# Kernel tuning notes

Hardware: AMD Instinct MI355X
Metric: run time of the kernel (lower is better)

Reference implementation:

```python
import jax, jax.numpy as jnp
import numpy as np

N, L, LEADS = 512, 640, 3
COND_DIM, NUM_K, DIM_K = 1, 100, 5
FLAT = 256 * 79  # 20224, from conv stack trace


def _leaky(x):
    return jnp.where(x >= 0, x, 0.2 * x)


def _sn(w, u):
    # PyTorch spectral_norm: one power iteration (u, v detached), sigma = u^T W v
    wm = w.reshape(w.shape[0], -1)
    v = wm.T @ u
    v = v / (jnp.linalg.norm(v) + 1e-12)
    u2 = wm @ v
    u2 = u2 / (jnp.linalg.norm(u2) + 1e-12)
    u2 = jax.lax.stop_gradient(u2)
    v = jax.lax.stop_gradient(v)
    sigma = u2 @ (wm @ v)
    return w / sigma


def _conv1d(x, w, b, stride, pad):
    y = jax.lax.conv_general_dilated(
        x, w, window_strides=(stride,), padding=[(pad, pad)],
        dimension_numbers=('NCH', 'OIH', 'NCH'))
    return y + b[None, :, None]


def setup_inputs() -> dict:
    key = jax.random.key(0)
    ks = jax.random.split(key, 16)
    g = lambda k, shp, s: (jax.random.normal(k, shp, dtype=jnp.float32) * s)
    inp = {
        'ecg': jax.random.normal(ks[0], (N, L, LEADS), dtype=jnp.float32),
        'condition': jax.random.randint(ks[1], (N, 1), 0, 4),
        'w1': g(ks[2], (64, LEADS, 5), 0.2), 'b1': jnp.zeros((64,), jnp.float32),
        'u1': jax.random.normal(ks[3], (64,), dtype=jnp.float32),
        'w2': g(ks[4], (128, 64, 7), 0.05), 'b2': jnp.zeros((128,), jnp.float32),
        'u2': jax.random.normal(ks[5], (128,), dtype=jnp.float32),
        'w3': g(ks[6], (256, 128, 9), 0.03), 'b3': jnp.zeros((256,), jnp.float32),
        'u3': jax.random.normal(ks[7], (256,), dtype=jnp.float32),
        'emb': g(ks[8], (4, COND_DIM), 1.0),
        'cond_w': g(ks[9], (50, COND_DIM), 0.5), 'cond_b': jnp.zeros((50,), jnp.float32),
        'mb_w': g(ks[10], (FLAT, NUM_K * DIM_K), 0.01),
        'fc_w': g(ks[11], (1, FLAT + NUM_K + 50), 0.01), 'fc_b': jnp.zeros((1,), jnp.float32),
    }
    return inp


def reference(ecg, condition, w1, b1, u1, w2, b2, u2, w3, b3, u3,
              emb, cond_w, cond_b, mb_w, fc_w, fc_b):
    # condition embedding -> Linear(cond_dim, 50)
    cemb = emb[condition[:, 0]]                       # [N, cond_dim]
    cond = cemb @ cond_w.T + cond_b                   # [N, 50]

    x = ecg.transpose(0, 2, 1)                        # [N, 3, 640]
    x = _leaky(_conv1d(x, _sn(w1, u1), b1, 2, 4))     # [N, 64, 322]
    x = _leaky(_conv1d(x, _sn(w2, u2), b2, 2, 3))     # [N, 128, 161]
    x = _leaky(_conv1d(x, _sn(w3, u3), b3, 2, 2))     # [N, 256, 79]
    flat = x.reshape(x.shape[0], -1)                  # [N, 20224]

    # minibatch discrimination
    act = (flat @ mb_w).reshape(-1, NUM_K, DIM_K)     # [N, K, D]
    l1 = jnp.abs(act[:, None] - act[None, :]).sum(-1)  # [N, N, K]
    feats = jnp.exp(-l1).sum(axis=1)                  # [N, K]

    out = jnp.concatenate([flat, feats, cond], axis=1)
    return out @ fc_w.T + fc_b                        # [N, 1]
```

## Files before the change

kernel.cpp:

```cpp
#include <hip/hip_runtime.h>
#include <math.h>

#define NB 512
#define LIN 640
#define NLEADS 3
#define L1O 322
#define L2O 161
#define L3O 79
#define C1N 64
#define C2N 128
#define C3N 256
#define FLATSZ 20224
#define NUMK 100
#define DIMK 5
#define SPLITK 16

typedef __attribute__((ext_vector_type(8))) short short8;
typedef __attribute__((ext_vector_type(4))) float f32x4;

__device__ __forceinline__ unsigned short f2bf(float x){
  unsigned u = __builtin_bit_cast(unsigned, x);
  unsigned r = u + 0x7FFFu + ((u >> 16) & 1u);
  return (unsigned short)(r >> 16);
}
__device__ __forceinline__ float bf2f(unsigned short x){
  unsigned u = ((unsigned)x) << 16;
  return __builtin_bit_cast(float, u);
}

__device__ __forceinline__ float block_reduce_sum(float val, float* red){
#pragma unroll
  for(int off=32; off>0; off>>=1) val += __shfl_down(val, off, 64);
  int lane = threadIdx.x & 63;
  int wv = threadIdx.x >> 6;
  if(lane==0) red[wv] = val;
  __syncthreads();
  int nw = blockDim.x >> 6;
  float r = red[0];
  for(int i=1;i<nw;i++) r += red[i];
  __syncthreads();
  return r;
}

__global__ __launch_bounds__(256)
void sn_pass1(const float* __restrict__ w1, const float* __restrict__ u1,
              const float* __restrict__ w2, const float* __restrict__ u2,
              const float* __restrict__ w3, const float* __restrict__ u3,
              float* __restrict__ v_all, float* __restrict__ ss){
  __shared__ float red[4];
  int b = blockIdx.x, tid = threadIdx.x;
  const float* w; const float* u; int O, C, off, c, widx;
  if(b==0){ w=w1; u=u1; O=64;  C=15;   off=0;   c=tid;            widx=0; }
  else if(b<3){ w=w2; u=u2; O=128; C=448; off=16;  c=(b-1)*256+tid; widx=1; }
  else { w=w3; u=u3; O=256; C=1152; off=464; c=(b-3)*256+tid;      widx=2; }
  float vv = 0.f;
  if(c < C){
    for(int o=0;o<O;o+=4){
      vv += w[(o+0)*C+c]*u[o+0] + w[(o+1)*C+c]*u[o+1]
          + w[(o+2)*C+c]*u[o+2] + w[(o+3)*C+c]*u[o+3];
    }
    v_all[off + c] = vv;
  }
  float ps = (c < C) ? vv*vv : 0.f;
  float tot = block_reduce_sum(ps, red);
  if(tid==0) atomicAdd(&ss[widx], tot);
}

__global__ __launch_bounds__(256)
void sn_pass2(const float* __restrict__ w1, const float* __restrict__ w2,
              const float* __restrict__ w3, const float* __restrict__ v_all,
              float* __restrict__ Sun){
  int b = blockIdx.x, tid = threadIdx.x;
  int lane = tid & 63, wv = tid >> 6;
  const float* w; int C, off, o, widx;
  if(b < 16){ w=w1; C=15;   off=0;   o=b*4+wv;      widx=0; }
  else if(b < 48){ w=w2; C=448; off=16;  o=(b-16)*4+wv; widx=1; }
  else { w=w3; C=1152; off=464; o=(b-48)*4+wv;          widx=2; }
  float t = 0.f;
  for(int c=lane; c<C; c+=64) t += w[o*C+c]*v_all[off+c];
#pragma unroll
  for(int s=32; s>0; s>>=1) t += __shfl_down(t, s, 64);
  if(lane==0) atomicAdd(&Sun[widx], t*t);
}

__global__ void sn_final(const float* __restrict__ ss, const float* __restrict__ Sun,
                         float* __restrict__ scale){
  int tid = threadIdx.x;
  if(tid < 3){
    float inv = 1.f/(sqrtf(ss[tid])+1e-12f);
    float S = Sun[tid]*inv*inv;
    scale[tid] = (sqrtf(S)+1e-12f)/S;
  }
}

__global__ void wprep_kernel(const float* __restrict__ w1, const float* __restrict__ w2,
                             const float* __restrict__ w3, const float* __restrict__ scale,
                             unsigned short* __restrict__ w1p, unsigned short* __restrict__ w2p,
                             unsigned short* __restrict__ w3p){
  int idx = blockIdx.x*256 + threadIdx.x;
  float s1 = scale[0], s2 = scale[1], s3 = scale[2];
  if(idx < C1N*32){
    int o = idx >> 5, kk = idx & 31;
    w1p[idx] = (kk < 15) ? f2bf(w1[o*15+kk]*s1) : 0;
  }
  if(idx < C2N*448){
    int o = idx / 448, k2 = idx - o*448;
    int r = k2 >> 6, i = k2 & 63;
    w2p[idx] = f2bf(w2[o*448 + i*7 + r]*s2);
  }
  if(idx < C3N*1152){
    int o = idx / 1152, k2 = idx - o*1152;
    int r = k2 >> 7, i = k2 & 127;
    w3p[idx] = f2bf(w3[o*1152 + i*9 + r]*s3);
  }
}

__global__ __launch_bounds__(256, 2)
void conv123_mfma(const float* __restrict__ ecg, const unsigned short* __restrict__ w1p,
                  const float* __restrict__ b1, const unsigned short* __restrict__ w2p,
                  const float* __restrict__ b2, const unsigned short* __restrict__ w3p,
                  const float* __restrict__ b3, unsigned short* __restrict__ flatbf){
  __shared__ unsigned short y2buf[22712];
  __shared__ unsigned short slabs[13600];
  __shared__ unsigned short B1s[3584];
  int n = blockIdx.x, tid = threadIdx.x;
  int lane = tid & 63, w = tid >> 6;

  if(tid < 136){
    y2buf[tid] = 0;
    y2buf[82*136 + tid] = 0;
    y2buf[83*136 + tid] = 0;
    y2buf[11424 + tid] = 0;
    y2buf[11424 + 81*136 + tid] = 0;
    y2buf[11424 + 82*136 + tid] = 0;
  }

  const float* eb = ecg + (size_t)n*LIN*NLEADS;
  f32x4 zero4 = {0.f,0.f,0.f,0.f};

  for(int tile=0; tile<2; tile++){
    int c0    = tile ? 189 : 0;
    int tbase = tile ? 96  : 0;
    int suboff= tile ? -94 : 2;

    __syncthreads();
    {
      uint4 z = {0u,0u,0u,0u};
      uint4* zd = (uint4*)slabs;
#pragma unroll
      for(int q=0;q<7;q++){
        int f = q*256 + tid;
        if(f < 1700) zd[f] = z;
      }
    }

    short8 a1 = *(const short8*)(w1p + ((w*16 + (lane&15))<<5) + (lane>>4)*8);
#pragma unroll
    for(int half=0; half<2; half++){
      const int tp0 = half*112;
      const int nt0 = half*7;
      const int ntc = half ? 6 : 7;
      const int rows = half ? 96 : 112;
      __syncthreads();
      for(int q=0;q<14;q++){
        int e = q*256 + tid;
        if(e < rows*32){
          int tpl = e >> 5, kk = e & 31;
          unsigned short v = 0;
          if(kk < 15){
            int i = kk/5, r = kk - i*5;
            int p = 2*(c0 + tp0 + tpl) - 4 + r;
            if((unsigned)p < (unsigned)LIN) v = f2bf(eb[p*NLEADS + i]);
          }
          B1s[tpl*32 + kk] = v;
        }
      }
      __syncthreads();
      f32x4 c1[7];
      for(int j=0;j<ntc;j++){
        short8 b = *(const short8*)(B1s + ((((nt0+j)*16 + (lane&15)) - tp0)<<5) + (lane>>4)*8);
        c1[j] = __builtin_amdgcn_mfma_f32_16x16x32_bf16(a1, b, zero4, 0, 0, 0);
      }
#pragma unroll
      for(int reg=0;reg<4;reg++){
        int o = w*16 + (lane>>4)*4 + reg;
        float bias = b1[o];
        for(int j=0;j<ntc;j++){
          int tp = (nt0+j)*16 + (lane&15);
          int t1 = c0 + tp;
          int sub = (t1>>1) + suboff;
          if(t1 < L1O && sub < 100){
            float v = c1[j][reg] + bias;
            v = v>=0.f ? v : 0.2f*v;
            slabs[((t1&1)?6800:0) + sub*68 + o] = f2bf(v);
          }
        }
      }
    }
    __syncthreads();

    f32x4 acc[2][6];
#pragma unroll
    for(int i=0;i<2;i++)
#pragma unroll
      for(int j=0;j<6;j++) acc[i][j] = zero4;

    const unsigned short* w2base = w2p + ((size_t)(w*2*16 + (lane&15)))*448 + (lane>>4)*8;
    short8 a_cur[2];
    a_cur[0] = *(const short8*)(w2base);
    a_cur[1] = *(const short8*)(w2base + 16*448);

    for(int ck=0; ck<14; ck++){
      short8 a_nxt[2];
      if(ck < 13){
        a_nxt[0] = *(const short8*)(w2base + (ck+1)*32);
        a_nxt[1] = *(const short8*)(w2base + 16*448 + (ck+1)*32);
      }
      int r = ck >> 1, i0 = (ck & 1)*32;
      int p = (r+1) & 1;
      int m = ((r-3) - p) >> 1;
      int base = (p?6800:0) + (m+2 + (lane&15))*68 + i0 + (lane>>4)*8;
      short8 b[6];
#pragma unroll
      for(int nt=0;nt<6;nt++)
        b[nt] = *(const short8*)(slabs + base + nt*16*68);
#pragma unroll
      for(int mm=0;mm<2;mm++)
#pragma unroll
        for(int nt=0;nt<6;nt++)
          acc[mm][nt] = __builtin_amdgcn_mfma_f32_16x16x32_bf16(a_cur[mm], b[nt], acc[mm][nt], 0, 0, 0);
      if(ck < 13){ a_cur[0] = a_nxt[0]; a_cur[1] = a_nxt[1]; }
    }

#pragma unroll
    for(int mm=0;mm<2;mm++){
#pragma unroll
      for(int reg=0;reg<4;reg++){
        int o = (w*2+mm)*16 + (lane>>4)*4 + reg;
        float bias = b2[o];
#pragma unroll
        for(int nt=0;nt<6;nt++){
          int tl = nt*16 + (lane&15);
          int t = tbase + tl;
          if(t < L2O){
            float v = acc[mm][nt][reg] + bias;
            v = v>=0.f ? v : 0.2f*v;
            y2buf[((t&1)?11424:0) + ((t>>1)+1)*136 + o] = f2bf(v);
          }
        }
      }
    }
  }
  __syncthreads();

  f32x4 acc3[4][5];
#pragma unroll
  for(int i=0;i<4;i++)
#pragma unroll
    for(int j=0;j<5;j++) acc3[i][j] = zero4;

  const unsigned short* wbase = w3p + ((size_t)(w*64) + (lane&15))*1152 + (lane>>4)*8;
  short8 abuf[3][4];
#pragma unroll
  for(int d=0; d<2; d++)
#pragma unroll
    for(int mm=0;mm<4;mm++)
      abuf[d][mm] = *(const short8*)(wbase + mm*16*1152 + d*32);

#pragma unroll
  for(int ck=0; ck<36; ck++){
    const int cur = ck % 3;
    const int nxt = (ck+2) % 3;
    if(ck+2 < 36){
      int kc = (ck+2)*32;
#pragma unroll
      for(int mm=0;mm<4;mm++)
        abuf[nxt][mm] = *(const short8*)(wbase + mm*16*1152 + kc);
    }
    int r = ck >> 2, i0 = (ck & 3) * 32;
    int cbase = ((r & 1) ? 11424 : 0) + (r >> 1)*136 + i0 + (lane>>4)*8;
    short8 b[5];
#pragma unroll
    for(int nt=0;nt<5;nt++){
      int t = nt*16 + (lane&15);
      b[nt] = *(const short8*)(y2buf + cbase + t*136);
    }
#pragma unroll
    for(int mm=0;mm<4;mm++)
#pragma unroll
      for(int nt=0;nt<5;nt++)
        acc3[mm][nt] = __builtin_amdgcn_mfma_f32_16x16x32_bf16(abuf[cur][mm], b[nt], acc3[mm][nt], 0, 0, 0);
  }
#pragma unroll
  for(int mm=0;mm<4;mm++){
#pragma unroll
    for(int reg=0;reg<4;reg++){
      int o = w*64 + mm*16 + (lane>>4)*4 + reg;
      float bias = b3[o];
#pragma unroll
      for(int nt=0;nt<5;nt++){
        int t = nt*16 + (lane&15);
        if(t < L3O){
          float v = acc3[mm][nt][reg] + bias;
          v = v>=0.f ? v : 0.2f*v;
          flatbf[(size_t)n*FLATSZ + o*L3O + t] = f2bf(v);
        }
      }
    }
  }
}

__global__ __launch_bounds__(256)
void mbw_transpose(const float* __restrict__ mbw, unsigned short* __restrict__ mbwT){
  __shared__ unsigned short tile[32][36];
  int k0 = blockIdx.x*32, n0 = blockIdx.y*32, tid = threadIdx.x;
  int r = tid >> 3, c4 = (tid & 7) * 4;
  int nbase = n0 + c4;
  if(nbase + 3 < 500){
    float4 v = *(const float4*)(mbw + (size_t)(k0+r)*500 + nbase);
    tile[r][c4+0] = f2bf(v.x);
    tile[r][c4+1] = f2bf(v.y);
    tile[r][c4+2] = f2bf(v.z);
    tile[r][c4+3] = f2bf(v.w);
  } else {
#pragma unroll
    for(int j=0;j<4;j++){
      int nn = nbase + j;
      float v = (nn < 500) ? mbw[(size_t)(k0+r)*500 + nn] : 0.f;
      tile[r][c4+j] = f2bf(v);
    }
  }
  __syncthreads();
  int nl = tid >> 3, kq = (tid & 7) * 4;
  unsigned short t0 = tile[kq+0][nl], t1 = tile[kq+1][nl];
  unsigned short t2 = tile[kq+2][nl], t3 = tile[kq+3][nl];
  uint2 p;
  p.x = (unsigned)t0 | ((unsigned)t1 << 16);
  p.y = (unsigned)t2 | ((unsigned)t3 << 16);
  *(uint2*)(mbwT + (size_t)(n0+nl)*FLATSZ + k0 + kq) = p;
}

__global__ __launch_bounds__(256)
void mb_gemm_mfma(const unsigned short* __restrict__ flatbf, const unsigned short* __restrict__ mbwT,
                  float* __restrict__ part){
  __shared__ unsigned short As[64*32];
  __shared__ unsigned short Bs[64*32];
  int tid = threadIdx.x;
  int lane = tid & 63, w = tid >> 6;
  int m0 = blockIdx.x*64, n0 = blockIdx.y*64, bz = blockIdx.z;
  int t_start = bz*39 + (bz<8 ? bz : 8);
  int t_count = 39 + (bz<8 ? 1 : 0);
  int k0 = t_start*32;
  f32x4 zero = {0.f,0.f,0.f,0.f};
  f32x4 acc[4];
#pragma unroll
  for(int i=0;i<4;i++) acc[i] = zero;
  int arow = tid >> 2, acol = (tid & 3) * 8;
  for(int t=0; t<t_count; t++, k0+=32){
    __syncthreads();
    ((uint4*)As)[tid] = *(const uint4*)(flatbf + (size_t)(m0+arow)*FLATSZ + k0 + acol);
    ((uint4*)Bs)[tid] = *(const uint4*)(mbwT  + (size_t)(n0+arow)*FLATSZ + k0 + acol);
    __syncthreads();
    short8 a = *(const short8*)(As + (w*16 + (lane&15))*32 + (lane>>4)*8);
#pragma unroll
    for(int nt=0;nt<4;nt++){
      short8 b = *(const short8*)(Bs + (nt*16 + (lane&15))*32 + (lane>>4)*8);
      acc[nt] = __builtin_amdgcn_mfma_f32_16x16x32_bf16(a, b, acc[nt], 0, 0, 0);
    }
  }
  float* po = part + (size_t)bz*NB*500;
#pragma unroll
  for(int nt=0;nt<4;nt++){
#pragma unroll
    for(int reg=0;reg<4;reg++){
      int m = m0 + w*16 + (lane>>4)*4 + reg;
      int c = n0 + nt*16 + (lane&15);
      if(c < 500) po[(size_t)m*500 + c] = acc[nt][reg];
    }
  }
}

__global__ void mb_reduce_kernel(const float* __restrict__ part, float* __restrict__ actT){
  int idx = blockIdx.x*256 + threadIdx.x;
  float s = 0.f;
#pragma unroll
  for(int z=0;z<SPLITK;z++) s += part[(size_t)z*NB*500 + idx];
  int n = idx/500, c = idx - n*500;
  actT[(size_t)c*NB + n] = s;
}

__global__ __launch_bounds__(256)
void feats_kernel(const float* __restrict__ actT, float* __restrict__ feats){
  __shared__ float ash[4][50];
  __shared__ float pred[4][4];
  int i0 = blockIdx.x*4, k0 = blockIdx.y*10;
  int tid = threadIdx.x, lane = tid & 63, wv = tid >> 6;
  if(tid < 200){
    int ii = tid/50, c = tid - ii*50;
    ash[ii][c] = actT[(size_t)(k0*5+c)*NB + i0 + ii];
  }
  __syncthreads();
  const float LOG2E = 1.4426950408889634f;
  int j1 = tid, j2 = tid + 256;
  for(int kk=0; kk<10; kk++){
    const float* r0 = actT + (size_t)(k0+kk)*5*NB;
    float xa0=r0[j1], xa1=r0[NB+j1], xa2=r0[2*NB+j1], xa3=r0[3*NB+j1], xa4=r0[4*NB+j1];
    float xb0=r0[j2], xb1=r0[NB+j2], xb2=r0[2*NB+j2], xb3=r0[3*NB+j2], xb4=r0[4*NB+j2];
    float f[4];
#pragma unroll
    for(int ii=0; ii<4; ii++){
      float a0=ash[ii][kk*5+0], a1=ash[ii][kk*5+1], a2=ash[ii][kk*5+2],
            a3=ash[ii][kk*5+3], a4=ash[ii][kk*5+4];
      float la = fabsf(xa0-a0)+fabsf(xa1-a1)+fabsf(xa2-a2)+fabsf(xa3-a3)+fabsf(xa4-a4);
      float lb = fabsf(xb0-a0)+fabsf(xb1-a1)+fabsf(xb2-a2)+fabsf(xb3-a3)+fabsf(xb4-a4);
      f[ii] = exp2f(-LOG2E*la) + exp2f(-LOG2E*lb);
    }
#pragma unroll
    for(int ii=0; ii<4; ii++){
      float v = f[ii];
#pragma unroll
      for(int s=32; s>0; s>>=1) v += __shfl_down(v, s, 64);
      if(lane==0) pred[wv][ii] = v;
    }
    __syncthreads();
    if(tid < 4){
      float v = pred[0][tid] + pred[1][tid] + pred[2][tid] + pred[3][tid];
      feats[(size_t)(i0+tid)*NUMK + k0 + kk] = v;
    }
    __syncthreads();
  }
}

__global__ void final_kernel(const unsigned short* __restrict__ flatbf, const float* __restrict__ feats,
                             const int* __restrict__ condition, const float* __restrict__ emb,
                             const float* __restrict__ cond_w, const float* __restrict__ cond_b,
                             const float* __restrict__ fc_w, const float* __restrict__ fc_b,
                             float* __restrict__ out){
  __shared__ float red[4];
  int n = blockIdx.x, tid = threadIdx.x;
  float s = 0.f;
  const unsigned short* fr = flatbf + (size_t)n*FLATSZ;
  for(int q=tid; q<FLATSZ/8; q+=256){
    uint4 u = *(const uint4*)(fr + q*8);
    float4 wa = *(const float4*)(fc_w + q*8);
    float4 wb = *(const float4*)(fc_w + q*8 + 4);
    s += bf2f((unsigned short)(u.x & 0xffff))*wa.x + bf2f((unsigned short)(u.x >> 16))*wa.y
       + bf2f((unsigned short)(u.y & 0xffff))*wa.z + bf2f((unsigned short)(u.y >> 16))*wa.w
       + bf2f((unsigned short)(u.z & 0xffff))*wb.x + bf2f((unsigned short)(u.z >> 16))*wb.y
       + bf2f((unsigned short)(u.w & 0xffff))*wb.z + bf2f((unsigned short)(u.w >> 16))*wb.w;
  }
  for(int k=tid;k<NUMK;k+=256) s += feats[n*NUMK+k]*fc_w[FLATSZ+k];
  float ce = emb[condition[n]];
  for(int j=tid;j<50;j+=256) s += (ce*cond_w[j]+cond_b[j])*fc_w[FLATSZ+NUMK+j];
  s = block_reduce_sum(s, red);
  if(tid==0) out[n] = s + fc_b[0];
}

extern "C" void kernel_launch(void* const* d_in, const int* in_sizes, int n_in,
                              void* d_out, int out_size, void* d_ws, size_t ws_size,
                              hipStream_t stream) {
  const float* ecg   = (const float*)d_in[0];
  const int*   cond  = (const int*)  d_in[1];
  const float* w1    = (const float*)d_in[2];
  const float* b1    = (const float*)d_in[3];
  const float* u1    = (const float*)d_in[4];
  const float* w2    = (const float*)d_in[5];
  const float* b2    = (const float*)d_in[6];
  const float* u2    = (const float*)d_in[7];
  const float* w3    = (const float*)d_in[8];
  const float* b3    = (const float*)d_in[9];
  const float* u3    = (const float*)d_in[10];
  const float* emb   = (const float*)d_in[11];
  const float* condw = (const float*)d_in[12];
  const float* condb = (const float*)d_in[13];
  const float* mbw   = (const float*)d_in[14];
  const float* fcw   = (const float*)d_in[15];
  const float* fcb   = (const float*)d_in[16];

  float* ws = (float*)d_ws;
  float* scale = ws;
  float* ssbuf = ws + 16;
  float* Sunbuf= ws + 24;
  float* v_all = ws + 32;
  unsigned short* w1p  = (unsigned short*)(ws + 1648);
  unsigned short* w2p  = (unsigned short*)(ws + 2672);
  unsigned short* w3p  = (unsigned short*)(ws + 31344);
  unsigned short* mbwT = (unsigned short*)(ws + 178800);
  float* part  = ws + 5454448;
  float* actT  = ws + 9550448;
  float* feats = ws + 9806448;
  unsigned short* flatbf = (unsigned short*)(ws + 9857648);

  hipMemsetAsync((char*)d_ws + 64, 0, 64, stream);
  sn_pass1<<<8, 256, 0, stream>>>(w1,u1,w2,u2,w3,u3, v_all, ssbuf);
  sn_pass2<<<112, 256, 0, stream>>>(w1,w2,w3, v_all, Sunbuf);
  sn_final<<<1, 64, 0, stream>>>(ssbuf, Sunbuf, scale);
  wprep_kernel<<<1152, 256, 0, stream>>>(w1, w2, w3, scale, w1p, w2p, w3p);
  conv123_mfma<<<NB, 256, 0, stream>>>(ecg, w1p, b1, w2p, b2, w3p, b3, flatbf);
  mbw_transpose<<<dim3(632,16), 256, 0, stream>>>(mbw, mbwT);
  mb_gemm_mfma<<<dim3(8,8,SPLITK), 256, 0, stream>>>(flatbf, mbwT, part);
  mb_reduce_kernel<<<1000, 256, 0, stream>>>(part, actT);
  feats_kernel<<<dim3(128,10), 256, 0, stream>>>(actT, feats);
  final_kernel<<<NB, 256, 0, stream>>>(flatbf, feats, cond, emb, condw, condb, fcw, fcb, (float*)d_out);
}
```

Baseline: 307.7 us.

## Fold sn_final into wprep, compact conv1 staging, add MFMA priority, halve split-K

Several unrelated changes land together. The spectral-norm scale is now computed inside wprep_kernel, which removes the sn_final launch. Conv1 input staging packs each output position's 15 taps into a 16-element row in one pass, replacing two half-tile loads, and zero-fills the unused K fragment. s_setprio is raised around the MFMA loops in conv2 and conv3. The minibatch GEMM's split-K factor goes from 16 to 8, which halves partial-sum traffic but also halves the grid parallelism of that GEMM, and mb_reduce must match the new SPLITK.

```diff
diff --git a/kernel.cpp b/kernel.cpp
--- a/kernel.cpp
+++ b/kernel.cpp
@@ -13,7 +13,7 @@
 #define FLATSZ 20224
 #define NUMK 100
 #define DIMK 5
-#define SPLITK 16
+#define SPLITK 8
 
 typedef __attribute__((ext_vector_type(8))) short short8;
 typedef __attribute__((ext_vector_type(4))) float f32x4;
@@ -83,35 +83,32 @@
   if(lane==0) atomicAdd(&Sun[widx], t*t);
 }
 
-__global__ void sn_final(const float* __restrict__ ss, const float* __restrict__ Sun,
-                         float* __restrict__ scale){
-  int tid = threadIdx.x;
-  if(tid < 3){
-    float inv = 1.f/(sqrtf(ss[tid])+1e-12f);
-    float S = Sun[tid]*inv*inv;
-    scale[tid] = (sqrtf(S)+1e-12f)/S;
-  }
-}
-
 __global__ void wprep_kernel(const float* __restrict__ w1, const float* __restrict__ w2,
-                             const float* __restrict__ w3, const float* __restrict__ scale,
+                             const float* __restrict__ w3, const float* __restrict__ ss,
+                             const float* __restrict__ Sun,
                              unsigned short* __restrict__ w1p, unsigned short* __restrict__ w2p,
                              unsigned short* __restrict__ w3p){
+  float sc[3];
+#pragma unroll
+  for(int i=0;i<3;i++){
+    float inv = 1.f/(sqrtf(ss[i])+1e-12f);
+    float S = Sun[i]*inv*inv;
+    sc[i] = (sqrtf(S)+1e-12f)/S;
+  }
   int idx = blockIdx.x*256 + threadIdx.x;
-  float s1 = scale[0], s2 = scale[1], s3 = scale[2];
   if(idx < C1N*32){
     int o = idx >> 5, kk = idx & 31;
-    w1p[idx] = (kk < 15) ? f2bf(w1[o*15+kk]*s1) : 0;
+    w1p[idx] = (kk < 15) ? f2bf(w1[o*15+kk]*sc[0]) : 0;
   }
   if(idx < C2N*448){
     int o = idx / 448, k2 = idx - o*448;
     int r = k2 >> 6, i = k2 & 63;
-    w2p[idx] = f2bf(w2[o*448 + i*7 + r]*s2);
+    w2p[idx] = f2bf(w2[o*448 + i*7 + r]*sc[1]);
   }
   if(idx < C3N*1152){
     int o = idx / 1152, k2 = idx - o*1152;
     int r = k2 >> 7, i = k2 & 127;
-    w3p[idx] = f2bf(w3[o*1152 + i*9 + r]*s3);
+    w3p[idx] = f2bf(w3[o*1152 + i*9 + r]*sc[2]);
   }
 }
 
@@ -122,7 +119,7 @@
                   const float* __restrict__ b3, unsigned short* __restrict__ flatbf){
   __shared__ unsigned short y2buf[22712];
   __shared__ unsigned short slabs[13600];
-  __shared__ unsigned short B1s[3584];
+  __shared__ unsigned short B1s[3328];
   int n = blockIdx.x, tid = threadIdx.x;
   int lane = tid & 63, w = tid >> 6;
 
@@ -153,46 +150,61 @@
         if(f < 1700) zd[f] = z;
       }
     }
-
-    short8 a1 = *(const short8*)(w1p + ((w*16 + (lane&15))<<5) + (lane>>4)*8);
-#pragma unroll
-    for(int half=0; half<2; half++){
-      const int tp0 = half*112;
-      const int nt0 = half*7;
-      const int ntc = half ? 6 : 7;
-      const int rows = half ? 96 : 112;
-      __syncthreads();
-      for(int q=0;q<14;q++){
-        int e = q*256 + tid;
-        if(e < rows*32){
-          int tpl = e >> 5, kk = e & 31;
-          unsigned short v = 0;
-          if(kk < 15){
-            int i = kk/5, r = kk - i*5;
-            int p = 2*(c0 + tp0 + tpl) - 4 + r;
-            if((unsigned)p < (unsigned)LIN) v = f2bf(eb[p*NLEADS + i]);
-          }
-          B1s[tpl*32 + kk] = v;
+    if(tid < 208){
+      int t1 = c0 + tid;
+      int p0 = 2*t1 - 4;
+      unsigned short row16[16];
+      row16[15] = 0;
+      if(p0 >= 0 && p0 <= 635){
+        const float* f = eb + p0*NLEADS;
+#pragma unroll
+        for(int rp=0; rp<5; rp++)
+#pragma unroll
+          for(int i=0;i<3;i++)
+            row16[i*5+rp] = f2bf(f[3*rp+i]);
+      } else {
+#pragma unroll
+        for(int rp=0; rp<5; rp++){
+          int p = p0 + rp;
+          bool ok = (unsigned)p < (unsigned)LIN;
+#pragma unroll
+          for(int i=0;i<3;i++)
+            row16[i*5+rp] = ok ? f2bf(eb[p*NLEADS+i]) : (unsigned short)0;
         }
       }
-      __syncthreads();
-      f32x4 c1[7];
-      for(int j=0;j<ntc;j++){
-        short8 b = *(const short8*)(B1s + ((((nt0+j)*16 + (lane&15)) - tp0)<<5) + (lane>>4)*8);
-        c1[j] = __builtin_amdgcn_mfma_f32_16x16x32_bf16(a1, b, zero4, 0, 0, 0);
-      }
-#pragma unroll
-      for(int reg=0;reg<4;reg++){
-        int o = w*16 + (lane>>4)*4 + reg;
-        float bias = b1[o];
+      unsigned* dst = (unsigned*)(B1s + tid*16);
+#pragma unroll
+      for(int q=0;q<8;q++)
+        dst[q] = (unsigned)row16[2*q] | ((unsigned)row16[2*q+1] << 16);
+    }
+    __syncthreads();
+
+    {
+      short8 a1 = *(const short8*)(w1p + ((w*16 + (lane&15))<<5) + (lane>>4)*8);
+      int cfrag = lane >> 4;
+#pragma unroll
+      for(int half=0; half<2; half++){
+        int nt0 = half*7, ntc = half ? 6 : 7;
+        f32x4 c1[7];
         for(int j=0;j<ntc;j++){
           int tp = (nt0+j)*16 + (lane&15);
-          int t1 = c0 + tp;
-          int sub = (t1>>1) + suboff;
-          if(t1 < L1O && sub < 100){
-            float v = c1[j][reg] + bias;
-            v = v>=0.f ? v : 0.2f*v;
-            slabs[((t1&1)?6800:0) + sub*68 + o] = f2bf(v);
+          short8 b = {0,0,0,0,0,0,0,0};
+          if(cfrag < 2) b = *(const short8*)(B1s + tp*16 + cfrag*8);
+          c1[j] = __builtin_amdgcn_mfma_f32_16x16x32_bf16(a1, b, zero4, 0, 0, 0);
+        }
+#pragma unroll
+        for(int reg=0;reg<4;reg++){
+          int o = w*16 + (lane>>4)*4 + reg;
+          float bias = b1[o];
+          for(int j=0;j<ntc;j++){
+            int tp = (nt0+j)*16 + (lane&15);
+            int t1 = c0 + tp;
+            int sub = (t1>>1) + suboff;
+            if(t1 < L1O && sub < 100){
+              float v = c1[j][reg] + bias;
+              v = v>=0.f ? v : 0.2f*v;
+              slabs[((t1&1)?6800:0) + sub*68 + o] = f2bf(v);
+            }
           }
         }
       }
@@ -224,11 +236,13 @@
 #pragma unroll
       for(int nt=0;nt<6;nt++)
         b[nt] = *(const short8*)(slabs + base + nt*16*68);
+      __builtin_amdgcn_s_setprio(1);
 #pragma unroll
       for(int mm=0;mm<2;mm++)
 #pragma unroll
         for(int nt=0;nt<6;nt++)
           acc[mm][nt] = __builtin_amdgcn_mfma_f32_16x16x32_bf16(a_cur[mm], b[nt], acc[mm][nt], 0, 0, 0);
+      __builtin_amdgcn_s_setprio(0);
       if(ck < 13){ a_cur[0] = a_nxt[0]; a_cur[1] = a_nxt[1]; }
     }
 
@@ -285,11 +299,13 @@
       int t = nt*16 + (lane&15);
       b[nt] = *(const short8*)(y2buf + cbase + t*136);
     }
+    __builtin_amdgcn_s_setprio(1);
 #pragma unroll
     for(int mm=0;mm<4;mm++)
 #pragma unroll
       for(int nt=0;nt<5;nt++)
         acc3[mm][nt] = __builtin_amdgcn_mfma_f32_16x16x32_bf16(abuf[cur][mm], b[nt], acc3[mm][nt], 0, 0, 0);
+    __builtin_amdgcn_s_setprio(0);
   }
 #pragma unroll
   for(int mm=0;mm<4;mm++){
@@ -348,9 +364,8 @@
   int tid = threadIdx.x;
   int lane = tid & 63, w = tid >> 6;
   int m0 = blockIdx.x*64, n0 = blockIdx.y*64, bz = blockIdx.z;
-  int t_start = bz*39 + (bz<8 ? bz : 8);
-  int t_count = 39 + (bz<8 ? 1 : 0);
-  int k0 = t_start*32;
+  int t_count = 79;
+  int k0 = bz*79*32;
   f32x4 zero = {0.f,0.f,0.f,0.f};
   f32x4 acc[4];
 #pragma unroll
@@ -478,7 +493,6 @@
   const float* fcb   = (const float*)d_in[16];
 
   float* ws = (float*)d_ws;
-  float* scale = ws;
   float* ssbuf = ws + 16;
   float* Sunbuf= ws + 24;
   float* v_all = ws + 32;
@@ -494,8 +508,7 @@
   hipMemsetAsync((char*)d_ws + 64, 0, 64, stream);
   sn_pass1<<<8, 256, 0, stream>>>(w1,u1,w2,u2,w3,u3, v_all, ssbuf);
   sn_pass2<<<112, 256, 0, stream>>>(w1,w2,w3, v_all, Sunbuf);
-  sn_final<<<1, 64, 0, stream>>>(ssbuf, Sunbuf, scale);
-  wprep_kernel<<<1152, 256, 0, stream>>>(w1, w2, w3, scale, w1p, w2p, w3p);
+  wprep_kernel<<<1152, 256, 0, stream>>>(w1, w2, w3, ssbuf, Sunbuf, w1p, w2p, w3p);
   conv123_mfma<<<NB, 256, 0, stream>>>(ecg, w1p, b1, w2p, b2, w3p, b3, flatbf);
   mbw_transpose<<<dim3(632,16), 256, 0, stream>>>(mbw, mbwT);
   mb_gemm_mfma<<<dim3(8,8,SPLITK), 256, 0, stream>>>(flatbf, mbwT, part);
```

Measured after the change: 309.0 us. No clear change (+0.4%).
